# Kernel optimization log

Measured on AMD Instinct MI355X. Metric: run time of the kernel, lower is better.

## Reference

```python
import jax, jax.numpy as jnp
import numpy as np

UNITS = 1024
IN_DIM = 512
BATCH = 64
SEQ = 512


def setup_inputs() -> dict:
    key = jax.random.key(0)
    k1, k2, k3, k4 = jax.random.split(key, 4)
    x = jax.random.normal(k1, (BATCH, SEQ, IN_DIM), dtype=jnp.float32)
    # Keras LSTM params: kernel [D,4U], recurrent_kernel [U,4U], bias [4U]; gate order i,f,c,o
    Wx = jax.random.normal(k2, (IN_DIM, 4 * UNITS), dtype=jnp.float32) * (1.0 / np.sqrt(IN_DIM))
    Wh = jax.random.normal(k3, (UNITS, 4 * UNITS), dtype=jnp.float32) * (1.0 / np.sqrt(UNITS))
    b = jnp.zeros((4 * UNITS,), dtype=jnp.float32).at[UNITS:2 * UNITS].set(1.0)  # unit_forget_bias
    return {"x": x, "Wx": Wx, "Wh": Wh, "b": b}


def reference(x, Wx, Wh, b):
    B, T, D = x.shape
    U = Wh.shape[0]
    # Precompute input projections for all timesteps in one GEMM: [B,T,4U]
    gx = jnp.einsum('btd,dg->btg', x, Wx) + b
    gx = jnp.swapaxes(gx, 0, 1)  # [T,B,4U] for scan

    def step(carry, gx_t):
        h, c = carry
        g = gx_t + h @ Wh  # [B,4U]
        i, f, cc, o = jnp.split(g, 4, axis=-1)
        i = jax.nn.sigmoid(i)
        f = jax.nn.sigmoid(f)
        o = jax.nn.sigmoid(o)
        c_new = f * c + i * jnp.tanh(cc)
        h_new = o * jnp.tanh(c_new)
        return (h_new, c_new), None

    h0 = jnp.zeros((B, U), dtype=x.dtype)
    c0 = jnp.zeros((B, U), dtype=x.dtype)
    (h, c), _ = jax.lax.scan(step, (h0, c0), gx)
    # Keras return_state LSTM: pred (last output) == h_state
    return jnp.concatenate([h, h, c], axis=-1)
```

## Files before the change

kernel.cpp:

```cpp
#include <hip/hip_runtime.h>
#include <stdint.h>

#define T_STEPS 512
#define RING 16
#define SLOT_SHORTS 65536

typedef short short8 __attribute__((ext_vector_type(8)));
typedef float f32x16 __attribute__((ext_vector_type(16)));

#define OFF_DONE 0
#define DONE_BYTES (512 * 2 * 4 * 64)
#define OFF_HRING DONE_BYTES
#define OFF_XF (OFF_HRING + RING * SLOT_SHORTS * 2)
#define XF_BYTES (512 * 2 * 4 * 8 * 64 * 8 * 2)
#define OFF_WPACK (OFF_XF + XF_BYTES)
#define MEMSET_BYTES (OFF_HRING + SLOT_SHORTS * 2)

#define W_STR 1544
#define G_STR 36

__device__ __forceinline__ unsigned short f2bf(float f) {
  unsigned u = __float_as_uint(f);
  u += 0x7fffu + ((u >> 16) & 1u);
  return (unsigned short)(u >> 16);
}

__global__ __launch_bounds__(256) void k_xpack(const float* __restrict__ x,
                                               unsigned short* __restrict__ xf) {
  int o = blockIdx.x * 256 + threadIdx.x;
  int lane = o & 63;
  int kk = (o >> 6) & 7;
  int ks = (o >> 9) & 3;
  int g = (o >> 11) & 1;
  int t = o >> 12;
  int n = lane & 31, hh = lane >> 5;
  const float* src = x + (((size_t)(g * 32 + n) * 512 + t) * 512 +
                          ks * 128 + kk * 16 + hh * 8);
  float4 v0 = *(const float4*)src;
  float4 v1 = *(const float4*)(src + 4);
  short8 w;
  w[0] = (short)f2bf(v0.x); w[1] = (short)f2bf(v0.y);
  w[2] = (short)f2bf(v0.z); w[3] = (short)f2bf(v0.w);
  w[4] = (short)f2bf(v1.x); w[5] = (short)f2bf(v1.y);
  w[6] = (short)f2bf(v1.z); w[7] = (short)f2bf(v1.w);
  *(short8*)(xf + (size_t)o * 8) = w;
}

__global__ __launch_bounds__(256) void k_wpack(const float* __restrict__ Wx,
                                               const float* __restrict__ Wh,
                                               unsigned short* __restrict__ wp) {
  __shared__ unsigned short tile[64 * 68];
  int tid = threadIdx.x, lane = tid & 63, wave = tid >> 6;
  int kt = blockIdx.x >> 6;
  int ct = blockIdx.x & 63;
  int K0 = kt * 64, C0 = ct * 64;
  const float* src = (K0 < 512) ? (Wx + (size_t)K0 * 4096)
                                : (Wh + (size_t)(K0 - 512) * 4096);
  #pragma unroll
  for (int i = 0; i < 16; ++i) {
    int kl = i * 4 + wave;
    float v = src[(size_t)kl * 4096 + C0 + lane];
    tile[lane * 68 + kl] = f2bf(v);
  }
  __syncthreads();
  #pragma unroll
  for (int i = 0; i < 16; ++i) {
    int c = i * 4 + wave;
    int col = C0 + c;
    int gg = col >> 10, idx = col & 1023;
    int cp = (idx >> 3) * 32 + gg * 8 + (idx & 7);
    wp[(size_t)cp * 1536 + K0 + lane] = tile[c * 68 + lane];
  }
}

__global__ __launch_bounds__(256, 1) void k_scan(
    const unsigned short* __restrict__ xf,
    const unsigned short* __restrict__ wp,
    const float* __restrict__ bias,
    float* __restrict__ out,
    unsigned* __restrict__ done,
    unsigned short* __restrict__ hring) {
  __shared__ __align__(16) unsigned short Wlds[32 * W_STR];
  __shared__ float Gs[4][32 * G_STR];

  const int tid = threadIdx.x;
  const int lane = tid & 63;
  const int ks = tid >> 6;
  const int bid = blockIdx.x;
  const int g = bid & 1;
  const int cb = bid >> 1;
  const int cohort = cb >> 4;
  const int n = lane & 31;
  const int hh = lane >> 5;

  for (int i = tid; i < 32 * 192; i += 256) {
    int row = i / 192, o = i % 192;
    *(short8*)&Wlds[row * W_STR + o * 8] =
        *(const short8*)&wp[((size_t)cb * 32 + row) * 1536 + o * 8];
  }

  const int m = tid >> 3, uu = tid & 7;
  const int ug = cb * 8 + uu;
  const float bi = bias[ug], bff = bias[1024 + ug];
  const float bc_ = bias[2048 + ug], bo = bias[3072 + ug];
  float c_state = 0.f;
  const int ksp = cb >> 5, kkp = (cb >> 1) & 15, hhp = cb & 1;
  __syncthreads();

  const unsigned short* wb = &Wlds[n * W_STR + hh * 8];

  #pragma unroll 1
  for (int t = 0; t < T_STEPS; ++t) {
    f32x16 acc;
    #pragma unroll
    for (int r = 0; r < 16; ++r) acc[r] = 0.f;

    {
      const unsigned short* xs =
          xf + ((((size_t)t * 2 + g) * 4 + ks) * 8) * 512 + lane * 8;
      #pragma unroll
      for (int kk = 0; kk < 8; ++kk) {
        short8 xa = *(const short8*)(xs + kk * 512);
        short8 b = *(const short8*)(wb + ks * 128 + kk * 16);
        acc = __builtin_amdgcn_mfma_f32_32x32x16_bf16(xa, b, acc, 0, 0, 0);
      }
    }

    if (t > 0 && lane == 0) {
      const unsigned long long* dp = (const unsigned long long*)(
          done + (((size_t)(t - 1) * 2 + g) * 4 + ks) * 16);
      float burn = c_state + 1.0f;
      while (__hip_atomic_load(dp, __ATOMIC_RELAXED,
                               __HIP_MEMORY_SCOPE_AGENT) != 0x0000001000000010ULL) {
        #pragma unroll
        for (int i = 0; i < 64; ++i)
          burn = __builtin_fmaf(burn, 1.0000001f, 1e-30f);
      }
      asm volatile("" :: "v"(burn));
    }
    __builtin_amdgcn_fence(__ATOMIC_ACQUIRE, "workgroup");
    if (t > 0 && (t & (RING - 1)) == 0)
      __builtin_amdgcn_fence(__ATOMIC_ACQUIRE, "agent");

    {
      const unsigned short* hs = hring + (size_t)(t & (RING - 1)) * SLOT_SHORTS +
                                 ((g * 4 + ks) * 16) * 512 + lane * 8;
      short8 ha[16];
      #pragma unroll
      for (int kk = 0; kk < 16; ++kk)
        ha[kk] = *(const short8*)(hs + kk * 512);
      #pragma unroll
      for (int kk = 0; kk < 16; ++kk) {
        short8 b = *(const short8*)(wb + 512 + ks * 256 + kk * 16);
        acc = __builtin_amdgcn_mfma_f32_32x32x16_bf16(ha[kk], b, acc, 0, 0, 0);
      }
    }

    #pragma unroll
    for (int r = 0; r < 16; ++r) {
      int row = (r & 3) + 8 * (r >> 2) + 4 * hh;
      Gs[ks][row * G_STR + n] = acc[r];
    }
    __syncthreads();

    float sI = bi, sF = bff, sC = bc_, sO = bo;
    #pragma unroll
    for (int w = 0; w < 4; ++w) {
      sI += Gs[w][m * G_STR + uu];
      sF += Gs[w][m * G_STR + 8 + uu];
      sC += Gs[w][m * G_STR + 16 + uu];
      sO += Gs[w][m * G_STR + 24 + uu];
    }
    float ig = 1.f / (1.f + __expf(-sI));
    float fg = 1.f / (1.f + __expf(-sF));
    float og = 1.f / (1.f + __expf(-sO));
    float cb2 = tanhf(sC);
    c_state = fg * c_state + ig * cb2;
    float h = og * tanhf(c_state);

    unsigned hv = (unsigned)f2bf(h);
    unsigned o1 = (unsigned)__shfl_xor((int)hv, 1, 64);
    unsigned lo = hv | (o1 << 16);
    unsigned long long hi = (unsigned long long)(unsigned)__shfl_xor((int)lo, 2, 64);
    unsigned long long v64 = ((unsigned long long)lo) | (hi << 32);
    if ((uu & 3) == 0) {
      unsigned short* hdst = hring + (size_t)((t + 1) & (RING - 1)) * SLOT_SHORTS +
                             ((g * 4 + ksp) * 16 + kkp) * 512 +
                             (hhp * 32 + m) * 8 + uu;
      __hip_atomic_store((unsigned long long*)hdst, v64,
                         __ATOMIC_RELAXED, __HIP_MEMORY_SCOPE_AGENT);
    }
    if (t == T_STEPS - 1) {
      float* orow = out + (size_t)(g * 32 + m) * 3072 + ug;
      orow[0] = h;
      orow[1024] = h;
      orow[2048] = c_state;
    }
    __syncthreads();
    if (tid == 0)
      __hip_atomic_fetch_add(
          done + (((size_t)t * 2 + g) * 4 + (cohort >> 1)) * 16 + (cohort & 1),
          1u, __ATOMIC_RELAXED, __HIP_MEMORY_SCOPE_AGENT);
  }
}

extern "C" void kernel_launch(void* const* d_in, const int* in_sizes, int n_in,
                              void* d_out, int out_size, void* d_ws, size_t ws_size,
                              hipStream_t stream) {
  const float* x  = (const float*)d_in[0];
  const float* Wx = (const float*)d_in[1];
  const float* Wh = (const float*)d_in[2];
  const float* b  = (const float*)d_in[3];
  float* out = (float*)d_out;
  char* ws = (char*)d_ws;
  unsigned* done = (unsigned*)(ws + OFF_DONE);
  unsigned short* hring = (unsigned short*)(ws + OFF_HRING);
  unsigned short* xf = (unsigned short*)(ws + OFF_XF);
  unsigned short* wp = (unsigned short*)(ws + OFF_WPACK);

  hipMemsetAsync(d_ws, 0, MEMSET_BYTES, stream);
  k_xpack<<<8192, 256, 0, stream>>>(x, xf);
  k_wpack<<<1536, 256, 0, stream>>>(Wx, Wh, wp);

  void* args[] = {(void*)&xf, (void*)&wp, (void*)&b, (void*)&out, (void*)&done,
                  (void*)&hring};
  hipLaunchCooperativeKernel((void*)k_scan, dim3(256), dim3(256), args, 0, stream);
}
```

Measured before the change: 2.292 ms.

## Repartition LSTM scan into batch groups with register-resident Wh and XCC-local sync

The scan is repartitioned so each block handles 8 batch rows and 32 units across all 1536 K. The recurrent weight slice is held in registers (64 short8 per lane), so each wave does the full K reduction and the LDS gate reduction and a syncthreads disappear. A startup handshake detects whether all blocks of a batch group sit on one XCC and, if so, uses non-coherent sc0 loads and workgroup-scope atomics for the per-step handoff, with an agent-scope fallback otherwise. Hidden-state loads are double-buffered against MFMAs, tanh is replaced by an exp-based form, and spin-waits use s_sleep instead of burn loops. It risks heavy register pressure and relies on an XCC-locality assumption for correctness of the fast path.

```diff
diff --git a/kernel.cpp b/kernel.cpp
--- a/kernel.cpp
+++ b/kernel.cpp
@@ -3,21 +3,21 @@
 
 #define T_STEPS 512
 #define RING 16
-#define SLOT_SHORTS 65536
 
 typedef short short8 __attribute__((ext_vector_type(8)));
 typedef float f32x16 __attribute__((ext_vector_type(16)));
 
-#define OFF_DONE 0
-#define DONE_BYTES (512 * 2 * 4 * 64)
-#define OFF_HRING DONE_BYTES
-#define OFF_XF (OFF_HRING + RING * SLOT_SHORTS * 2)
-#define XF_BYTES (512 * 2 * 4 * 8 * 64 * 8 * 2)
-#define OFF_WPACK (OFF_XF + XF_BYTES)
-#define MEMSET_BYTES (OFF_HRING + SLOT_SHORTS * 2)
-
-#define W_STR 1544
-#define G_STR 36
+#define OFF_HDR 0
+#define OFF_DONE 256
+#define DONE_BYTES (8 * 512 * 8 * 64)
+#define OFF_RING (OFF_DONE + DONE_BYTES)
+#define SLOT_BYTES (8 * 16384)
+#define RING_BYTES (RING * SLOT_BYTES)
+#define OFF_XF (OFF_RING + RING_BYTES)
+#define XF_BYTES (8 * 512 * 32 * 256)
+#define OFF_WP (OFF_XF + XF_BYTES)
+#define WP_BYTES (128 * 96 * 64 * 16)
+#define MEMSET_BYTES (OFF_RING + SLOT_BYTES)
 
 __device__ __forceinline__ unsigned short f2bf(float f) {
   unsigned u = __float_as_uint(f);
@@ -28,201 +28,317 @@
 __global__ __launch_bounds__(256) void k_xpack(const float* __restrict__ x,
                                                unsigned short* __restrict__ xf) {
   int o = blockIdx.x * 256 + threadIdx.x;
-  int lane = o & 63;
-  int kk = (o >> 6) & 7;
-  int ks = (o >> 9) & 3;
-  int g = (o >> 11) & 1;
-  int t = o >> 12;
-  int n = lane & 31, hh = lane >> 5;
-  const float* src = x + (((size_t)(g * 32 + n) * 512 + t) * 512 +
-                          ks * 128 + kk * 16 + hh * 8);
+  int kseg = o & 1;
+  int m = (o >> 1) & 7;
+  int kx = (o >> 4) & 31;
+  int t = (o >> 9) & 511;
+  int rg = (o >> 18) & 7;
+  const float* src = x + ((size_t)(rg * 8 + m) * 512 + t) * 512 + kx * 16 + kseg * 8;
   float4 v0 = *(const float4*)src;
   float4 v1 = *(const float4*)(src + 4);
-  short8 w;
-  w[0] = (short)f2bf(v0.x); w[1] = (short)f2bf(v0.y);
-  w[2] = (short)f2bf(v0.z); w[3] = (short)f2bf(v0.w);
-  w[4] = (short)f2bf(v1.x); w[5] = (short)f2bf(v1.y);
-  w[6] = (short)f2bf(v1.z); w[7] = (short)f2bf(v1.w);
-  *(short8*)(xf + (size_t)o * 8) = w;
+  short8 wv;
+  wv[0] = (short)f2bf(v0.x); wv[1] = (short)f2bf(v0.y);
+  wv[2] = (short)f2bf(v0.z); wv[3] = (short)f2bf(v0.w);
+  wv[4] = (short)f2bf(v1.x); wv[5] = (short)f2bf(v1.y);
+  wv[6] = (short)f2bf(v1.z); wv[7] = (short)f2bf(v1.w);
+  *(short8*)(xf + (size_t)o * 8) = wv;
 }
 
 __global__ __launch_bounds__(256) void k_wpack(const float* __restrict__ Wx,
                                                const float* __restrict__ Wh,
                                                unsigned short* __restrict__ wp) {
-  __shared__ unsigned short tile[64 * 68];
-  int tid = threadIdx.x, lane = tid & 63, wave = tid >> 6;
-  int kt = blockIdx.x >> 6;
-  int ct = blockIdx.x & 63;
-  int K0 = kt * 64, C0 = ct * 64;
-  const float* src = (K0 < 512) ? (Wx + (size_t)K0 * 4096)
-                                : (Wh + (size_t)(K0 - 512) * 4096);
-  #pragma unroll
-  for (int i = 0; i < 16; ++i) {
-    int kl = i * 4 + wave;
-    float v = src[(size_t)kl * 4096 + C0 + lane];
-    tile[lane * 68 + kl] = f2bf(v);
+  __shared__ float tile[128][32];
+  int tid = threadIdx.x;
+  int ch = blockIdx.x;
+  int ct = blockIdx.y;
+  int c = tid & 31, kl8 = tid >> 5;
+  int gate = c >> 3;
+  int co = gate * 1024 + ct * 8 + (c & 7);
+  const float* src;
+  int K0;
+  if (ch < 4) { src = Wx; K0 = ch * 128; }
+  else        { src = Wh; K0 = ch * 128 - 512; }
+#pragma unroll
+  for (int p = 0; p < 16; ++p) {
+    int row = p * 8 + kl8;
+    tile[row][c] = src[(size_t)(K0 + row) * 4096 + co];
   }
   __syncthreads();
-  #pragma unroll
-  for (int i = 0; i < 16; ++i) {
-    int c = i * 4 + wave;
-    int col = C0 + c;
-    int gg = col >> 10, idx = col & 1023;
-    int cp = (idx >> 3) * 32 + gg * 8 + (idx & 7);
-    wp[(size_t)cp * 1536 + K0 + lane] = tile[c * 68 + lane];
-  }
-}
+#pragma unroll
+  for (int h2 = 0; h2 < 2; ++h2) {
+    int line = h2 * 256 + tid;
+    int kt2 = line >> 6, l = line & 63;
+    short8 v;
+#pragma unroll
+    for (int j = 0; j < 8; ++j)
+      v[j] = (short)f2bf(tile[kt2 * 16 + (l >> 5) * 8 + j][l & 31]);
+    *(short8*)(wp + ((size_t)(ct * 96 + ch * 8 + kt2) * 64 + l) * 8) = v;
+  }
+}
+
+#define H_LDF(BUF, BASE)                                                         \
+  _Pragma("unroll") for (int j = 0; j < 8; ++j)                                  \
+      asm volatile("global_load_dwordx4 %0, %1, off sc0"                         \
+                   : "=v"(BUF[j]) : "v"(hb + (BASE + j) * 128));
+#define H_LDA(BUF, BASE)                                                         \
+  _Pragma("unroll") for (int j = 0; j < 8; ++j)                                  \
+      asm volatile("global_load_dwordx4 %0, %1, off sc0 sc1"                     \
+                   : "=v"(BUF[j]) : "v"(hb + (BASE + j) * 128));
+#define H_WAIT8 { asm volatile("s_waitcnt vmcnt(8)" ::: "memory");               \
+                  __builtin_amdgcn_sched_barrier(0); }
+#define H_WAIT0 { asm volatile("s_waitcnt vmcnt(0)" ::: "memory");               \
+                  __builtin_amdgcn_sched_barrier(0); }
+#define H_MM(BUF, BASE)                                                          \
+  _Pragma("unroll") for (int j = 0; j < 8; ++j)                                  \
+      acc = __builtin_amdgcn_mfma_f32_32x32x16_bf16(BUF[j], whf[BASE + j], acc,  \
+                                                    0, 0, 0);
 
 __global__ __launch_bounds__(256, 1) void k_scan(
     const unsigned short* __restrict__ xf,
     const unsigned short* __restrict__ wp,
     const float* __restrict__ bias,
     float* __restrict__ out,
+    unsigned* __restrict__ hdr,
     unsigned* __restrict__ done,
     unsigned short* __restrict__ hring) {
-  __shared__ __align__(16) unsigned short Wlds[32 * W_STR];
-  __shared__ float Gs[4][32 * G_STR];
+  __shared__ __align__(16) unsigned short Wlds[4][32][64][8];
 
   const int tid = threadIdx.x;
   const int lane = tid & 63;
-  const int ks = tid >> 6;
+  const int w = tid >> 6;
   const int bid = blockIdx.x;
-  const int g = bid & 1;
-  const int cb = bid >> 1;
-  const int cohort = cb >> 4;
-  const int n = lane & 31;
-  const int hh = lane >> 5;
-
-  for (int i = tid; i < 32 * 192; i += 256) {
-    int row = i / 192, o = i % 192;
-    *(short8*)&Wlds[row * W_STR + o * 8] =
-        *(const short8*)&wp[((size_t)cb * 32 + row) * 1536 + o * 8];
-  }
-
-  const int m = tid >> 3, uu = tid & 7;
-  const int ug = cb * 8 + uu;
-  const float bi = bias[ug], bff = bias[1024 + ug];
+  const int rg = bid & 7;
+  const int cm = bid >> 3;
+
+  for (int i = tid; i < 4 * 32 * 64; i += 256) {
+    int ww = i >> 11, r = i & 2047, kx = r >> 6, l = r & 63;
+    *(short8*)&Wlds[ww][kx][l][0] =
+        *(const short8*)(wp + (((size_t)(cm * 4 + ww) * 96 + kx) * 64 + l) * 8);
+  }
+  short8 whf[64];
+#pragma unroll
+  for (int kh = 0; kh < 64; ++kh)
+    whf[kh] = *(const short8*)(
+        wp + (((size_t)(cm * 4 + w) * 96 + 32 + kh) * 64 + lane) * 8);
+
+  if (tid == 0) {
+    unsigned xcc = 0;
+    asm volatile("s_getreg_b32 %0, hwreg(HW_REG_XCC_ID)" : "=s"(xcc));
+    __hip_atomic_fetch_or(hdr + rg, 1u << (xcc & 31u), __ATOMIC_RELAXED,
+                          __HIP_MEMORY_SCOPE_AGENT);
+    __hip_atomic_fetch_add(hdr + 16, 1u, __ATOMIC_RELEASE, __HIP_MEMORY_SCOPE_AGENT);
+  }
+  while (__hip_atomic_load(hdr + 16, __ATOMIC_ACQUIRE, __HIP_MEMORY_SCOPE_AGENT) <
+         256u)
+    __builtin_amdgcn_s_sleep(8);
+  const bool fastc =
+      (__popc(__hip_atomic_load(hdr + rg, __ATOMIC_RELAXED,
+                                __HIP_MEMORY_SCOPE_AGENT)) == 1);
+
+  if (fastc && lane == 0)
+    __hip_atomic_fetch_add(hdr + 32 + rg, 1u, __ATOMIC_RELAXED,
+                           __HIP_MEMORY_SCOPE_WORKGROUP);
+  __syncthreads();
+  if (tid == 0) {
+    int ok = 1;
+    if (fastc) {
+      unsigned v = 0;
+      int it = 0;
+      do {
+        asm volatile("global_load_dword %0, %1, off sc0\n\ts_waitcnt vmcnt(0)"
+                     : "=v"(v) : "v"(hdr + 32 + rg) : "memory");
+        if (v == 128u) break;
+        __builtin_amdgcn_s_sleep(8);
+      } while (++it < 30000);
+      ok = (v == 128u) ? 1 : 0;
+    }
+    if (!ok)
+      __hip_atomic_fetch_or(hdr + 48 + rg, 1u, __ATOMIC_RELAXED,
+                            __HIP_MEMORY_SCOPE_AGENT);
+    __hip_atomic_fetch_add(hdr + 17, 1u, __ATOMIC_RELEASE, __HIP_MEMORY_SCOPE_AGENT);
+  }
+  while (__hip_atomic_load(hdr + 17, __ATOMIC_ACQUIRE, __HIP_MEMORY_SCOPE_AGENT) <
+         256u)
+    __builtin_amdgcn_s_sleep(8);
+  const bool fastp =
+      fastc && (__hip_atomic_load(hdr + 48 + rg, __ATOMIC_RELAXED,
+                                  __HIP_MEMORY_SCOPE_AGENT) == 0u);
+  __syncthreads();
+
+  const int m = lane & 7;
+  const int uu = lane >> 3;
+  const int ug = cm * 32 + w * 8 + uu;
+  const float bi = bias[ug], bf_ = bias[1024 + ug];
   const float bc_ = bias[2048 + ug], bo = bias[3072 + ug];
+  const int r3 = m & 3;
+  const int sbase = ((m >> 2) & 1) * 32 + uu;
   float c_state = 0.f;
-  const int ksp = cb >> 5, kkp = (cb >> 1) & 15, hhp = cb & 1;
-  __syncthreads();
-
-  const unsigned short* wb = &Wlds[n * W_STR + hh * 8];
-
-  #pragma unroll 1
+
+  const unsigned short* xl = xf + (lane & 7) * 16 + (lane >> 5) * 8;
+  const unsigned short* wxl = (const unsigned short*)&Wlds[w][0][lane][0];
+  const int hcell = cm * 2 + (w >> 1);
+
+#pragma unroll 1
   for (int t = 0; t < T_STEPS; ++t) {
     f32x16 acc;
-    #pragma unroll
+#pragma unroll
     for (int r = 0; r < 16; ++r) acc[r] = 0.f;
 
     {
-      const unsigned short* xs =
-          xf + ((((size_t)t * 2 + g) * 4 + ks) * 8) * 512 + lane * 8;
-      #pragma unroll
-      for (int kk = 0; kk < 8; ++kk) {
-        short8 xa = *(const short8*)(xs + kk * 512);
-        short8 b = *(const short8*)(wb + ks * 128 + kk * 16);
-        acc = __builtin_amdgcn_mfma_f32_32x32x16_bf16(xa, b, acc, 0, 0, 0);
+      const unsigned short* xs = xl + (size_t)(rg * 512 + t) * 4096;
+#pragma unroll 8
+      for (int kx = 0; kx < 32; ++kx) {
+        short8 xa = *(const short8*)(xs + kx * 128);
+        short8 wb = *(const short8*)(wxl + kx * 512);
+        acc = __builtin_amdgcn_mfma_f32_32x32x16_bf16(xa, wb, acc, 0, 0, 0);
       }
     }
-
-    if (t > 0 && lane == 0) {
-      const unsigned long long* dp = (const unsigned long long*)(
-          done + (((size_t)(t - 1) * 2 + g) * 4 + ks) * 16);
-      float burn = c_state + 1.0f;
-      while (__hip_atomic_load(dp, __ATOMIC_RELAXED,
-                               __HIP_MEMORY_SCOPE_AGENT) != 0x0000001000000010ULL) {
-        #pragma unroll
-        for (int i = 0; i < 64; ++i)
-          burn = __builtin_fmaf(burn, 1.0000001f, 1e-30f);
+    asm volatile("s_waitcnt vmcnt(0)" ::: "memory");
+
+    if (t > 0) {
+      const unsigned* dp =
+          done + ((size_t)(rg * 512 + (t - 1)) * 8 + (lane & 7)) * 16;
+      unsigned v;
+      if (fastp) {
+        for (;;) {
+          asm volatile("global_load_dword %0, %1, off sc0\n\ts_waitcnt vmcnt(0)"
+                       : "=v"(v) : "v"(dp) : "memory");
+          if (__all(v == 16u)) break;
+          __builtin_amdgcn_s_sleep(1);
+        }
+      } else {
+        for (;;) {
+          v = __hip_atomic_load(dp, __ATOMIC_RELAXED, __HIP_MEMORY_SCOPE_AGENT);
+          if (__all(v == 16u)) break;
+          __builtin_amdgcn_s_sleep(2);
+        }
       }
-      asm volatile("" :: "v"(burn));
-    }
-    __builtin_amdgcn_fence(__ATOMIC_ACQUIRE, "workgroup");
-    if (t > 0 && (t & (RING - 1)) == 0)
-      __builtin_amdgcn_fence(__ATOMIC_ACQUIRE, "agent");
+    }
+    __builtin_amdgcn_sched_barrier(0);
 
     {
-      const unsigned short* hs = hring + (size_t)(t & (RING - 1)) * SLOT_SHORTS +
-                                 ((g * 4 + ks) * 16) * 512 + lane * 8;
-      short8 ha[16];
-      #pragma unroll
-      for (int kk = 0; kk < 16; ++kk)
-        ha[kk] = *(const short8*)(hs + kk * 512);
-      #pragma unroll
-      for (int kk = 0; kk < 16; ++kk) {
-        short8 b = *(const short8*)(wb + 512 + ks * 256 + kk * 16);
-        acc = __builtin_amdgcn_mfma_f32_32x32x16_bf16(ha[kk], b, acc, 0, 0, 0);
+      const unsigned short* hb = hring + (size_t)(t & (RING - 1)) * 65536 +
+                                 rg * 8192 + (lane & 7) * 16 + (lane >> 5) * 8;
+      short8 hA[8], hB[8];
+      if (fastp) {
+        H_LDF(hA, 0)  H_LDF(hB, 8)
+        H_WAIT8 H_MM(hA, 0)
+        H_LDF(hA, 16) H_WAIT8 H_MM(hB, 8)
+        H_LDF(hB, 24) H_WAIT8 H_MM(hA, 16)
+        H_LDF(hA, 32) H_WAIT8 H_MM(hB, 24)
+        H_LDF(hB, 40) H_WAIT8 H_MM(hA, 32)
+        H_LDF(hA, 48) H_WAIT8 H_MM(hB, 40)
+        H_LDF(hB, 56) H_WAIT8 H_MM(hA, 48)
+        H_WAIT0 H_MM(hB, 56)
+      } else {
+        H_LDA(hA, 0)  H_LDA(hB, 8)
+        H_WAIT8 H_MM(hA, 0)
+        H_LDA(hA, 16) H_WAIT8 H_MM(hB, 8)
+        H_LDA(hB, 24) H_WAIT8 H_MM(hA, 16)
+        H_LDA(hA, 32) H_WAIT8 H_MM(hB, 24)
+        H_LDA(hB, 40) H_WAIT8 H_MM(hA, 32)
+        H_LDA(hA, 48) H_WAIT8 H_MM(hB, 40)
+        H_LDA(hB, 56) H_WAIT8 H_MM(hA, 48)
+        H_WAIT0 H_MM(hB, 56)
       }
     }
 
-    #pragma unroll
-    for (int r = 0; r < 16; ++r) {
-      int row = (r & 3) + 8 * (r >> 2) + 4 * hh;
-      Gs[ks][row * G_STR + n] = acc[r];
-    }
-    __syncthreads();
-
-    float sI = bi, sF = bff, sC = bc_, sO = bo;
-    #pragma unroll
-    for (int w = 0; w < 4; ++w) {
-      sI += Gs[w][m * G_STR + uu];
-      sF += Gs[w][m * G_STR + 8 + uu];
-      sC += Gs[w][m * G_STR + 16 + uu];
-      sO += Gs[w][m * G_STR + 24 + uu];
-    }
+    float sg0, sg1, sg2, sg3;
+    {
+      float v0, v1, v2, v3;
+      v0 = __shfl(acc[0], sbase + 0, 64);  v1 = __shfl(acc[1], sbase + 0, 64);
+      v2 = __shfl(acc[2], sbase + 0, 64);  v3 = __shfl(acc[3], sbase + 0, 64);
+      sg0 = r3 == 0 ? v0 : r3 == 1 ? v1 : r3 == 2 ? v2 : v3;
+      v0 = __shfl(acc[0], sbase + 8, 64);  v1 = __shfl(acc[1], sbase + 8, 64);
+      v2 = __shfl(acc[2], sbase + 8, 64);  v3 = __shfl(acc[3], sbase + 8, 64);
+      sg1 = r3 == 0 ? v0 : r3 == 1 ? v1 : r3 == 2 ? v2 : v3;
+      v0 = __shfl(acc[0], sbase + 16, 64); v1 = __shfl(acc[1], sbase + 16, 64);
+      v2 = __shfl(acc[2], sbase + 16, 64); v3 = __shfl(acc[3], sbase + 16, 64);
+      sg2 = r3 == 0 ? v0 : r3 == 1 ? v1 : r3 == 2 ? v2 : v3;
+      v0 = __shfl(acc[0], sbase + 24, 64); v1 = __shfl(acc[1], sbase + 24, 64);
+      v2 = __shfl(acc[2], sbase + 24, 64); v3 = __shfl(acc[3], sbase + 24, 64);
+      sg3 = r3 == 0 ? v0 : r3 == 1 ? v1 : r3 == 2 ? v2 : v3;
+    }
+
+    float sI = sg0 + bi, sF = sg1 + bf_, sC = sg2 + bc_, sO = sg3 + bo;
     float ig = 1.f / (1.f + __expf(-sI));
     float fg = 1.f / (1.f + __expf(-sF));
     float og = 1.f / (1.f + __expf(-sO));
-    float cb2 = tanhf(sC);
-    c_state = fg * c_state + ig * cb2;
-    float h = og * tanhf(c_state);
+    float aC = fabsf(sC), eC = __expf(-2.f * aC);
+    float tC = __builtin_copysignf((1.f - eC) / (1.f + eC), sC);
+    c_state = fg * c_state + ig * tC;
+    float aH = fabsf(c_state), eH = __expf(-2.f * aH);
+    float th = __builtin_copysignf((1.f - eH) / (1.f + eH), c_state);
+    float h = og * th;
 
     unsigned hv = (unsigned)f2bf(h);
-    unsigned o1 = (unsigned)__shfl_xor((int)hv, 1, 64);
-    unsigned lo = hv | (o1 << 16);
-    unsigned long long hi = (unsigned long long)(unsigned)__shfl_xor((int)lo, 2, 64);
-    unsigned long long v64 = ((unsigned long long)lo) | (hi << 32);
-    if ((uu & 3) == 0) {
-      unsigned short* hdst = hring + (size_t)((t + 1) & (RING - 1)) * SLOT_SHORTS +
-                             ((g * 4 + ksp) * 16 + kkp) * 512 +
-                             (hhp * 32 + m) * 8 + uu;
-      __hip_atomic_store((unsigned long long*)hdst, v64,
-                         __ATOMIC_RELAXED, __HIP_MEMORY_SCOPE_AGENT);
+    unsigned p1 = (unsigned)__shfl_xor((int)hv, 8, 64);
+    unsigned lo = hv | (p1 << 16);
+    unsigned p2 = (unsigned)__shfl_xor((int)lo, 16, 64);
+    unsigned p3a = (unsigned)__shfl_xor((int)lo, 32, 64);
+    unsigned p3b = (unsigned)__shfl_xor((int)p2, 32, 64);
+    if (lane < 8) {
+      unsigned short* hd = hring + (size_t)((t + 1) & (RING - 1)) * 65536 +
+                           rg * 8192 + hcell * 128 + lane * 16 + (w & 1) * 8;
+      if (fastp) {
+        union { unsigned u[4]; short8 s; } pk;
+        pk.u[0] = lo; pk.u[1] = p2; pk.u[2] = p3a; pk.u[3] = p3b;
+        *(short8*)hd = pk.s;
+      } else {
+        unsigned long long a = ((unsigned long long)p2 << 32) | lo;
+        unsigned long long b2 = ((unsigned long long)p3b << 32) | p3a;
+        __hip_atomic_store((unsigned long long*)hd, a, __ATOMIC_RELAXED,
+                           __HIP_MEMORY_SCOPE_AGENT);
+        __hip_atomic_store(((unsigned long long*)hd) + 1, b2, __ATOMIC_RELAXED,
+                           __HIP_MEMORY_SCOPE_AGENT);
+      }
     }
     if (t == T_STEPS - 1) {
-      float* orow = out + (size_t)(g * 32 + m) * 3072 + ug;
+      float* orow = out + (size_t)(rg * 8 + m) * 3072 + ug;
       orow[0] = h;
       orow[1024] = h;
       orow[2048] = c_state;
     }
-    __syncthreads();
-    if (tid == 0)
-      __hip_atomic_fetch_add(
-          done + (((size_t)t * 2 + g) * 4 + (cohort >> 1)) * 16 + (cohort & 1),
-          1u, __ATOMIC_RELAXED, __HIP_MEMORY_SCOPE_AGENT);
+
+    asm volatile("s_waitcnt vmcnt(0)" ::: "memory");
+    if (lane == 0) {
+      unsigned* dadd = done + ((size_t)(rg * 512 + t) * 8 + (cm >> 2)) * 16;
+      if (fastp)
+        __hip_atomic_fetch_add(dadd, 1u, __ATOMIC_RELAXED,
+                               __HIP_MEMORY_SCOPE_WORKGROUP);
+      else
+        __hip_atomic_fetch_add(dadd, 1u, __ATOMIC_RELAXED,
+                               __HIP_MEMORY_SCOPE_AGENT);
+    }
+    __builtin_amdgcn_sched_barrier(0);
   }
 }
 
 extern "C" void kernel_launch(void* const* d_in, const int* in_sizes, int n_in,
                               void* d_out, int out_size, void* d_ws, size_t ws_size,
                               hipStream_t stream) {
-  const float* x  = (const float*)d_in[0];
+  (void)in_sizes; (void)n_in; (void)out_size; (void)ws_size;
+  const float* x = (const float*)d_in[0];
   const float* Wx = (const float*)d_in[1];
   const float* Wh = (const float*)d_in[2];
-  const float* b  = (const float*)d_in[3];
+  const float* b = (const float*)d_in[3];
   float* out = (float*)d_out;
   char* ws = (char*)d_ws;
+  unsigned* hdr = (unsigned*)(ws + OFF_HDR);
   unsigned* done = (unsigned*)(ws + OFF_DONE);
-  unsigned short* hring = (unsigned short*)(ws + OFF_HRING);
+  unsigned short* hring = (unsigned short*)(ws + OFF_RING);
   unsigned short* xf = (unsigned short*)(ws + OFF_XF);
-  unsigned short* wp = (unsigned short*)(ws + OFF_WPACK);
+  unsigned short* wp = (unsigned short*)(ws + OFF_WP);
 
   hipMemsetAsync(d_ws, 0, MEMSET_BYTES, stream);
   k_xpack<<<8192, 256, 0, stream>>>(x, xf);
-  k_wpack<<<1536, 256, 0, stream>>>(Wx, Wh, wp);
-
-  void* args[] = {(void*)&xf, (void*)&wp, (void*)&b, (void*)&out, (void*)&done,
-                  (void*)&hring};
-  hipLaunchCooperativeKernel((void*)k_scan, dim3(256), dim3(256), args, 0, stream);
-}
+  k_wpack<<<dim3(12, 128), 256, 0, stream>>>(Wx, Wh, wp);
+
+  void* args[] = {(void*)&xf, (void*)&wp, (void*)&b, (void*)&out,
+                  (void*)&hdr, (void*)&done, (void*)&hring};
+  hipError_t e = hipLaunchCooperativeKernel((void*)k_scan, dim3(256), dim3(256),
+                                            args, 0, stream);
+  if (e != hipSuccess) {
+    k_scan<<<dim3(256), dim3(256), 0, stream>>>(xf, wp, b, out, hdr, done, hring);
+  }
+}
```

Measured after the change: 5.766 ms. 2.52x slower.
